# Performance work log

Hardware: AMD Instinct MI355X
Metric: run time of the kernel (lower is better)

Reference implementation:

```python
import jax, jax.numpy as jnp
import numpy as np

NUM_NODES = 100000
NUM_EDGES = 1000000
NUM_REL = 3
NUM_GRAPHS = 512
VOCAB = 10000
EMBED_DIM = 64
HIDDEN_DIM = 64
NUM_CLS = 2


def setup_inputs() -> dict:
    key = jax.random.key(0)
    ks = jax.random.split(key, 10)
    x = jax.random.randint(ks[0], (NUM_NODES,), 0, VOCAB)
    edge_index = jax.random.randint(ks[1], (2, NUM_EDGES), 0, NUM_NODES)
    edge_type = jax.random.randint(ks[2], (NUM_EDGES,), 0, NUM_REL)
    batch = jnp.sort(jax.random.randint(ks[3], (NUM_NODES,), 0, NUM_GRAPHS))
    embed_table = jax.random.normal(ks[4], (VOCAB, EMBED_DIM), dtype=jnp.float32) * 0.02
    embed_table = embed_table.at[0].set(0.0)  # padding_idx=0
    W_rel = jax.random.normal(ks[5], (NUM_REL, EMBED_DIM, HIDDEN_DIM), dtype=jnp.float32) * 0.1
    W_root = jax.random.normal(ks[6], (EMBED_DIM, HIDDEN_DIM), dtype=jnp.float32) * 0.1
    conv_bias = jax.random.normal(ks[7], (HIDDEN_DIM,), dtype=jnp.float32) * 0.01
    lin_W = jax.random.normal(ks[8], (HIDDEN_DIM, NUM_CLS), dtype=jnp.float32) * 0.1
    lin_b = jnp.zeros((NUM_CLS,), dtype=jnp.float32)
    return {"x": x, "edge_index": edge_index, "edge_type": edge_type, "batch": batch,
            "embed_table": embed_table, "W_rel": W_rel, "W_root": W_root,
            "conv_bias": conv_bias, "lin_W": lin_W, "lin_b": lin_b}


def reference(x, edge_index, edge_type, batch, embed_table, W_rel, W_root, conv_bias, lin_W, lin_b):
    # Embedding lookup (padding row already zeroed)
    h = embed_table[x]                                   # [N, D]
    src, dst = edge_index[0], edge_index[1]
    # RGCNConv: root transform + per-relation mean-aggregated neighbor transform
    out = h @ W_root + conv_bias                          # [N, H]
    for r in range(NUM_REL):
        mask = (edge_type == r).astype(h.dtype)           # [E]
        hr = h @ W_rel[r]                                 # [N, H] tiny GEMM
        msg = hr[src] * mask[:, None]                     # [E, H] gather
        agg = jax.ops.segment_sum(msg, dst, num_segments=NUM_NODES)
        cnt = jax.ops.segment_sum(mask, dst, num_segments=NUM_NODES)
        out = out + agg / jnp.maximum(cnt, 1.0)[:, None]
    out = jax.nn.relu(out)
    # global_mean_pool over graph ids
    g_sum = jax.ops.segment_sum(out, batch, num_segments=NUM_GRAPHS)    # [G, H]
    g_cnt = jax.ops.segment_sum(jnp.ones_like(batch, dtype=out.dtype), batch, num_segments=NUM_GRAPHS)
    g_emb = g_sum / jnp.maximum(g_cnt, 1.0)[:, None]
    return g_emb @ lin_W + lin_b                          # [G, num_cls]
```

## Files before the change

### kernel.cpp

```cpp
#include <hip/hip_runtime.h>

#define N_NODES 100000
#define N_EDGES 1000000
#define N_GRAPHS 512
#define VOCAB 10000
#define DIM 64

#define NPB 64
#define NB 1563
#define EPB 4096
#define SB 245
#define BUILD_BLOCKS ((4 * VOCAB) / 16)
#define CAP 1152

typedef unsigned short ushort_t;

static __device__ __forceinline__ ushort_t f2bf(float f) {
    unsigned u = __float_as_uint(f);
    unsigned r = 0x7FFFu + ((u >> 16) & 1u);
    return (ushort_t)((u + r) >> 16);
}
#define BFLO(u) __uint_as_float((u) << 16)
#define BFHI(u) __uint_as_float((u) & 0xFFFF0000u)

__global__ __launch_bounds__(256)
void hist_build(const int* __restrict__ dst, int* __restrict__ bh,
                float* __restrict__ g_sum,
                const float* __restrict__ embed,
                const float* __restrict__ W_rel,
                const float* __restrict__ W_root,
                ushort_t* __restrict__ Tb) {
    if (blockIdx.x < SB) {
        for (int i = blockIdx.x * 256 + threadIdx.x; i < N_GRAPHS * DIM; i += SB * 256)
            g_sum[i] = 0.f;
        __shared__ int h[NB];
        for (int i = threadIdx.x; i < NB; i += 256) h[i] = 0;
        __syncthreads();
        int base = blockIdx.x * EPB;
        int lim  = base + EPB; if (lim > N_EDGES) lim = N_EDGES;
        for (int e = base + threadIdx.x; e < lim; e += 256)
            atomicAdd(&h[dst[e] >> 6], 1);
        __syncthreads();
        for (int i = threadIdx.x; i < NB; i += 256)
            bh[blockIdx.x * NB + i] = h[i];
    } else {
        int tid  = (blockIdx.x - SB) * 256 + threadIdx.x;
        int l    = tid & 63;
        int wave = tid >> 6;
        int sub  = l >> 4;
        int q    = l & 15;
        int row  = wave * 4 + sub;
        int m    = row / VOCAB;
        int v    = row - m * VOCAB;
        const float* W = (m == 0) ? W_root : (W_rel + (size_t)(m - 1) * DIM * DIM);
        float4 e4  = *(const float4*)(embed + (size_t)v * DIM + q * 4);
        float4 acc = {0.f, 0.f, 0.f, 0.f};
#pragma unroll
        for (int kk = 0; kk < 16; ++kk) {
            int srcl = sub * 16 + kk;
            float ex = __shfl(e4.x, srcl, 64);
            float ey = __shfl(e4.y, srcl, 64);
            float ez = __shfl(e4.z, srcl, 64);
            float ew = __shfl(e4.w, srcl, 64);
            const float4 w0 = *(const float4*)(W + (4 * kk + 0) * DIM + q * 4);
            const float4 w1 = *(const float4*)(W + (4 * kk + 1) * DIM + q * 4);
            const float4 w2 = *(const float4*)(W + (4 * kk + 2) * DIM + q * 4);
            const float4 w3 = *(const float4*)(W + (4 * kk + 3) * DIM + q * 4);
            acc.x += ex * w0.x; acc.y += ex * w0.y; acc.z += ex * w0.z; acc.w += ex * w0.w;
            acc.x += ey * w1.x; acc.y += ey * w1.y; acc.z += ey * w1.z; acc.w += ey * w1.w;
            acc.x += ez * w2.x; acc.y += ez * w2.y; acc.z += ez * w2.z; acc.w += ez * w2.w;
            acc.x += ew * w3.x; acc.y += ew * w3.y; acc.z += ew * w3.z; acc.w += ew * w3.w;
        }
        ushort_t* p = Tb + (size_t)row * DIM + q * 4;
        p[0] = f2bf(acc.x); p[1] = f2bf(acc.y);
        p[2] = f2bf(acc.z); p[3] = f2bf(acc.w);
    }
}

__global__ __launch_bounds__(256)
void rowscan(const int* __restrict__ bh, int* __restrict__ loc,
             int* __restrict__ btot) {
    __shared__ int wsum4[4];
    int b = blockIdx.x, t = threadIdx.x;
    int l = t & 63, wv = t >> 6;
    int v = (t < SB) ? bh[t * NB + b] : 0;
    int sc = v;
#pragma unroll
    for (int d = 1; d < 64; d <<= 1) {
        int tt = __shfl_up(sc, d, 64);
        if (l >= d) sc += tt;
    }
    if (l == 63) wsum4[wv] = sc;
    __syncthreads();
    if (t == 0) {
        int a = 0;
#pragma unroll
        for (int k = 0; k < 4; ++k) { int tmp = wsum4[k]; wsum4[k] = a; a += tmp; }
    }
    __syncthreads();
    int excl = sc - v + wsum4[wv];
    if (t < SB) loc[b * SB + t] = excl;
    if (t == 255) btot[b] = excl;
}

__global__ __launch_bounds__(512)
void bucket_scatter(const int* __restrict__ src,
                    const int* __restrict__ dst,
                    const int* __restrict__ etype,
                    const int* __restrict__ x,
                    const int* __restrict__ loc,
                    const int* __restrict__ btot,
                    int* __restrict__ bbase,
                    unsigned* __restrict__ rec) {
    __shared__ int wsum8[8];
    __shared__ int baseh[NB];
    __shared__ int h[NB];
    int t = threadIdx.x;
    int l = t & 63, wv = t >> 6;

    int v0 = (4 * t + 0 < NB) ? btot[4 * t + 0] : 0;
    int v1 = (4 * t + 1 < NB) ? btot[4 * t + 1] : 0;
    int v2 = (4 * t + 2 < NB) ? btot[4 * t + 2] : 0;
    int v3 = (4 * t + 3 < NB) ? btot[4 * t + 3] : 0;
    int lsum = v0 + v1 + v2 + v3;
    int sc = lsum;
#pragma unroll
    for (int d = 1; d < 64; d <<= 1) {
        int tt = __shfl_up(sc, d, 64);
        if (l >= d) sc += tt;
    }
    if (l == 63) wsum8[wv] = sc;
    __syncthreads();
    if (t == 0) {
        int a = 0;
#pragma unroll
        for (int k = 0; k < 8; ++k) { int tmp = wsum8[k]; wsum8[k] = a; a += tmp; }
    }
    __syncthreads();
    int p = sc - lsum + wsum8[wv];
    if (4 * t + 0 < NB) baseh[4 * t + 0] = p; p += v0;
    if (4 * t + 1 < NB) baseh[4 * t + 1] = p; p += v1;
    if (4 * t + 2 < NB) baseh[4 * t + 2] = p; p += v2;
    if (4 * t + 3 < NB) baseh[4 * t + 3] = p;
    __syncthreads();

    if (blockIdx.x == 0) {
        for (int i = t; i < NB; i += 512) bbase[i] = baseh[i];
        if (t == 0) bbase[NB] = N_EDGES;
    }
    for (int i = t; i < NB; i += 512) {
        baseh[i] += loc[i * SB + blockIdx.x];
        h[i] = 0;
    }
    __syncthreads();

    int base = blockIdx.x * EPB;
    int lim  = base + EPB; if (lim > N_EDGES) lim = N_EDGES;
    for (int e = base + t; e < lim; e += 512) {
        int d = dst[e];
        int b = d >> 6;
        int rk = atomicAdd(&h[b], 1);
        unsigned payload = ((unsigned)x[src[e]] << 8)
                         | ((unsigned)(d & 63) << 2)
                         | (unsigned)etype[e];
        rec[baseh[b] + rk] = payload;
    }
}

__global__ __launch_bounds__(256)
void sort_aggregate(const int* __restrict__ x,
                    const int* __restrict__ batch,
                    const int* __restrict__ bbase,
                    const unsigned* __restrict__ rec,
                    const ushort_t* __restrict__ Tb,
                    const float* __restrict__ bias,
                    float* __restrict__ g_sum) {
    __shared__ int cstart[257];
    __shared__ int cur[256];
    __shared__ int wsum4[4];
    __shared__ float inv_sh[256];
    __shared__ unsigned sortedc[CAP];
    __shared__ float rows[NPB * DIM];
    __shared__ float red[256];
    __shared__ int batch_sh[NPB];
    int b = blockIdx.x, t = threadIdx.x;
    int s = bbase[b];
    int e = bbase[b + 1];
    int ne = e - s;
    int nvalid = N_NODES - b * NPB; if (nvalid > NPB) nvalid = NPB;

    cstart[t] = 0;
    if (t < NPB) batch_sh[t] = (t < nvalid) ? batch[b * NPB + t] : -1;
    __syncthreads();
    for (int i = t; i < ne; i += 256)
        atomicAdd(&cstart[rec[s + i] & 0xFFu], 1);
    __syncthreads();
    {
        int l = t & 63, wv = t >> 6;
        int v = cstart[t];
        int sc = v;
#pragma unroll
        for (int d = 1; d < 64; d <<= 1) {
            int tt = __shfl_up(sc, d, 64);
            if (l >= d) sc += tt;
        }
        if (l == 63) wsum4[wv] = sc;
        __syncthreads();
        if (t == 0) {
            int a = 0;
#pragma unroll
            for (int k = 0; k < 4; ++k) { int tmp = wsum4[k]; wsum4[k] = a; a += tmp; }
        }
        __syncthreads();
        int excl = sc - v + wsum4[wv];
        __syncthreads();
        cstart[t] = excl;
        cur[t] = excl;
        if (t == 255) cstart[256] = excl + v;
    }
    __syncthreads();
    inv_sh[t] = 1.f / fmaxf((float)(cstart[t + 1] - cstart[t]), 1.f);
    for (int i = t; i < ne; i += 256) {
        unsigned p = rec[s + i];
        int rk = atomicAdd(&cur[p & 0xFFu], 1);
        sortedc[rk] = p;
    }
    __syncthreads();

    int grp = t >> 3;
    int sl  = t & 7;
    const ushort_t* TbRel = Tb + (size_t)VOCAB * DIM;
#pragma unroll
    for (int nn = 0; nn < 2; ++nn) {
        int n = grp * 2 + nn;
        if (n >= nvalid) continue;
        int node = b * NPB + n;
        int i0 = cstart[n << 2];
        int i1 = cstart[(n + 1) << 2];
        float a0 = 0.f, a1 = 0.f, a2 = 0.f, a3 = 0.f,
              a4 = 0.f, a5 = 0.f, a6 = 0.f, a7 = 0.f;
        int i = i0;
        for (; i + 4 <= i1; i += 4) {
            unsigned c1 = sortedc[i],     c2 = sortedc[i + 1];
            unsigned c3 = sortedc[i + 2], c4 = sortedc[i + 3];
            const uint4 t1 = *(const uint4*)(TbRel +
                ((size_t)(c1 & 3u) * VOCAB + (c1 >> 8)) * DIM + sl * 8);
            const uint4 t2 = *(const uint4*)(TbRel +
                ((size_t)(c2 & 3u) * VOCAB + (c2 >> 8)) * DIM + sl * 8);
            const uint4 t3 = *(const uint4*)(TbRel +
                ((size_t)(c3 & 3u) * VOCAB + (c3 >> 8)) * DIM + sl * 8);
            const uint4 t4 = *(const uint4*)(TbRel +
                ((size_t)(c4 & 3u) * VOCAB + (c4 >> 8)) * DIM + sl * 8);
            float iv1 = inv_sh[c1 & 0xFFu], iv2 = inv_sh[c2 & 0xFFu];
            float iv3 = inv_sh[c3 & 0xFFu], iv4 = inv_sh[c4 & 0xFFu];
            a0 += BFLO(t1.x) * iv1; a1 += BFHI(t1.x) * iv1;
            a2 += BFLO(t1.y) * iv1; a3 += BFHI(t1.y) * iv1;
            a4 += BFLO(t1.z) * iv1; a5 += BFHI(t1.z) * iv1;
            a6 += BFLO(t1.w) * iv1; a7 += BFHI(t1.w) * iv1;
            a0 += BFLO(t2.x) * iv2; a1 += BFHI(t2.x) * iv2;
            a2 += BFLO(t2.y) * iv2; a3 += BFHI(t2.y) * iv2;
            a4 += BFLO(t2.z) * iv2; a5 += BFHI(t2.z) * iv2;
            a6 += BFLO(t2.w) * iv2; a7 += BFHI(t2.w) * iv2;
            a0 += BFLO(t3.x) * iv3; a1 += BFHI(t3.x) * iv3;
            a2 += BFLO(t3.y) * iv3; a3 += BFHI(t3.y) * iv3;
            a4 += BFLO(t3.z) * iv3; a5 += BFHI(t3.z) * iv3;
            a6 += BFLO(t3.w) * iv3; a7 += BFHI(t3.w) * iv3;
            a0 += BFLO(t4.x) * iv4; a1 += BFHI(t4.x) * iv4;
            a2 += BFLO(t4.y) * iv4; a3 += BFHI(t4.y) * iv4;
            a4 += BFLO(t4.z) * iv4; a5 += BFHI(t4.z) * iv4;
            a6 += BFLO(t4.w) * iv4; a7 += BFHI(t4.w) * iv4;
        }
        for (; i < i1; ++i) {
            unsigned c1 = sortedc[i];
            const uint4 t1 = *(const uint4*)(TbRel +
                ((size_t)(c1 & 3u) * VOCAB + (c1 >> 8)) * DIM + sl * 8);
            float iv1 = inv_sh[c1 & 0xFFu];
            a0 += BFLO(t1.x) * iv1; a1 += BFHI(t1.x) * iv1;
            a2 += BFLO(t1.y) * iv1; a3 += BFHI(t1.y) * iv1;
            a4 += BFLO(t1.z) * iv1; a5 += BFHI(t1.z) * iv1;
            a6 += BFLO(t1.w) * iv1; a7 += BFHI(t1.w) * iv1;
        }
        int xv = x[node];
        const uint4 rt = *(const uint4*)(Tb + (size_t)xv * DIM + sl * 8);
        const float4 b0 = *(const float4*)(bias + sl * 8);
        const float4 b1 = *(const float4*)(bias + sl * 8 + 4);
        float* rp = rows + n * DIM + sl * 8;
        rp[0] = fmaxf(BFLO(rt.x) + b0.x + a0, 0.f);
        rp[1] = fmaxf(BFHI(rt.x) + b0.y + a1, 0.f);
        rp[2] = fmaxf(BFLO(rt.y) + b0.z + a2, 0.f);
        rp[3] = fmaxf(BFHI(rt.y) + b0.w + a3, 0.f);
        rp[4] = fmaxf(BFLO(rt.z) + b1.x + a4, 0.f);
        rp[5] = fmaxf(BFHI(rt.z) + b1.y + a5, 0.f);
        rp[6] = fmaxf(BFLO(rt.w) + b1.z + a6, 0.f);
        rp[7] = fmaxf(BFHI(rt.w) + b1.w + a7, 0.f);
    }
    __syncthreads();

    int gmin = batch_sh[0];
    int gmax = batch_sh[nvalid - 1];
    int f  = t & 63;
    int n0 = t >> 6;
    for (int g = gmin; g <= gmax; ++g) {
        float a = 0.f;
        for (int n = n0; n < nvalid; n += 4)
            a += (batch_sh[n] == g) ? rows[n * DIM + f] : 0.f;
        red[t] = a;
        __syncthreads();
        if (t < 64) {
            float tot = red[t] + red[t + 64] + red[t + 128] + red[t + 192];
            if (tot != 0.f) atomicAdd(&g_sum[g * DIM + t], tot);
        }
        __syncthreads();
    }
}

__device__ __forceinline__ int lbound(const int* __restrict__ b, int val) {
    int lo = 0, hi = N_NODES;
    while (lo < hi) {
        int mid = (lo + hi) >> 1;
        if (b[mid] < val) lo = mid + 1; else hi = mid;
    }
    return lo;
}

__global__ __launch_bounds__(64)
void final_linear(const int* __restrict__ batch,
                  const float* __restrict__ g_sum,
                  const float* __restrict__ lin_W,
                  const float* __restrict__ lin_b,
                  float* __restrict__ out) {
    int g = blockIdx.x;
    int l = threadIdx.x;
    int s = lbound(batch, g);
    int e = lbound(batch, g + 1);
    float mean = (e > s) ? g_sum[g * DIM + l] / (float)(e - s) : 0.f;
    float p0 = mean * lin_W[l * 2 + 0];
    float p1 = mean * lin_W[l * 2 + 1];
#pragma unroll
    for (int off2 = 32; off2 > 0; off2 >>= 1) {
        p0 += __shfl_down(p0, off2, 64);
        p1 += __shfl_down(p1, off2, 64);
    }
    if (l == 0) {
        out[g * 2 + 0] = p0 + lin_b[0];
        out[g * 2 + 1] = p1 + lin_b[1];
    }
}

extern "C" void kernel_launch(void* const* d_in, const int* in_sizes, int n_in,
                              void* d_out, int out_size, void* d_ws, size_t ws_size,
                              hipStream_t stream) {
    const int*   x      = (const int*)d_in[0];
    const int*   eidx   = (const int*)d_in[1];
    const int*   etype  = (const int*)d_in[2];
    const int*   batch  = (const int*)d_in[3];
    const float* embed  = (const float*)d_in[4];
    const float* W_rel  = (const float*)d_in[5];
    const float* W_root = (const float*)d_in[6];
    const float* bias   = (const float*)d_in[7];
    const float* lin_W  = (const float*)d_in[8];
    const float* lin_b  = (const float*)d_in[9];
    float* out = (float*)d_out;

    const int* src = eidx;
    const int* dst = eidx + N_EDGES;

    char* ws = (char*)d_ws;
    ushort_t* Tb    = (ushort_t*)(ws);
    unsigned* rec   = (unsigned*)(ws + 5120000);
    int* loc        = (int*)(ws + 9120000);
    int* btot       = (int*)(ws + 10651776);
    int* bbase      = (int*)(ws + 10658048);
    int* bh         = (int*)(ws + 10664320);
    float* g_sum    = (float*)(ws + 12196096);

    hist_build<<<SB + BUILD_BLOCKS, 256, 0, stream>>>(
        dst, bh, g_sum, embed, W_rel, W_root, Tb);

    rowscan<<<NB, 256, 0, stream>>>(bh, loc, btot);

    bucket_scatter<<<SB, 512, 0, stream>>>(src, dst, etype, x, loc, btot, bbase, rec);

    sort_aggregate<<<NB, 256, 0, stream>>>(x, batch, bbase, rec, Tb, bias, g_sum);

    final_linear<<<N_GRAPHS, 64, 0, stream>>>(batch, g_sum, lin_W, lin_b, out);
}
```

Baseline: 84.80 us.

## Precompute edge payloads in histogram pass and widen scatter blocks to 1024

Moves the x[src] gather and payload packing from bucket_scatter into hist_build, where it can overlap with the table-build blocks. The scatter then reads a precomputed payload array and runs with 1024 threads per block instead of 512. The intent is to shorten the serial scatter stage, which has only 245 blocks, by taking the random gather off its critical path. The cost is an extra 4 MB payload write and read through global memory, plus a larger workspace.

```diff
diff --git a/kernel.cpp b/kernel.cpp
--- a/kernel.cpp
+++ b/kernel.cpp
@@ -24,7 +24,12 @@
 #define BFHI(u) __uint_as_float((u) & 0xFFFF0000u)
 
 __global__ __launch_bounds__(256)
-void hist_build(const int* __restrict__ dst, int* __restrict__ bh,
+void hist_build(const int* __restrict__ src,
+                const int* __restrict__ dst,
+                const int* __restrict__ etype,
+                const int* __restrict__ x,
+                int* __restrict__ bh,
+                unsigned* __restrict__ payload,
                 float* __restrict__ g_sum,
                 const float* __restrict__ embed,
                 const float* __restrict__ W_rel,
@@ -38,8 +43,13 @@
         __syncthreads();
         int base = blockIdx.x * EPB;
         int lim  = base + EPB; if (lim > N_EDGES) lim = N_EDGES;
-        for (int e = base + threadIdx.x; e < lim; e += 256)
-            atomicAdd(&h[dst[e] >> 6], 1);
+        for (int e = base + threadIdx.x; e < lim; e += 256) {
+            int d = dst[e];
+            atomicAdd(&h[d >> 6], 1);
+            payload[e] = ((unsigned)x[src[e]] << 8)
+                       | ((unsigned)(d & 63) << 2)
+                       | (unsigned)etype[e];
+        }
         __syncthreads();
         for (int i = threadIdx.x; i < NB; i += 256)
             bh[blockIdx.x * NB + i] = h[i];
@@ -103,52 +113,46 @@
     if (t == 255) btot[b] = excl;
 }
 
-__global__ __launch_bounds__(512)
-void bucket_scatter(const int* __restrict__ src,
-                    const int* __restrict__ dst,
-                    const int* __restrict__ etype,
-                    const int* __restrict__ x,
+__global__ __launch_bounds__(1024)
+void bucket_scatter(const int* __restrict__ dst,
+                    const unsigned* __restrict__ payload,
                     const int* __restrict__ loc,
                     const int* __restrict__ btot,
                     int* __restrict__ bbase,
                     unsigned* __restrict__ rec) {
-    __shared__ int wsum8[8];
+    __shared__ int wsum16[16];
     __shared__ int baseh[NB];
     __shared__ int h[NB];
     int t = threadIdx.x;
     int l = t & 63, wv = t >> 6;
 
-    int v0 = (4 * t + 0 < NB) ? btot[4 * t + 0] : 0;
-    int v1 = (4 * t + 1 < NB) ? btot[4 * t + 1] : 0;
-    int v2 = (4 * t + 2 < NB) ? btot[4 * t + 2] : 0;
-    int v3 = (4 * t + 3 < NB) ? btot[4 * t + 3] : 0;
-    int lsum = v0 + v1 + v2 + v3;
+    int v0 = (2 * t + 0 < NB) ? btot[2 * t + 0] : 0;
+    int v1 = (2 * t + 1 < NB) ? btot[2 * t + 1] : 0;
+    int lsum = v0 + v1;
     int sc = lsum;
 #pragma unroll
     for (int d = 1; d < 64; d <<= 1) {
         int tt = __shfl_up(sc, d, 64);
         if (l >= d) sc += tt;
     }
-    if (l == 63) wsum8[wv] = sc;
+    if (l == 63) wsum16[wv] = sc;
     __syncthreads();
     if (t == 0) {
         int a = 0;
 #pragma unroll
-        for (int k = 0; k < 8; ++k) { int tmp = wsum8[k]; wsum8[k] = a; a += tmp; }
-    }
-    __syncthreads();
-    int p = sc - lsum + wsum8[wv];
-    if (4 * t + 0 < NB) baseh[4 * t + 0] = p; p += v0;
-    if (4 * t + 1 < NB) baseh[4 * t + 1] = p; p += v1;
-    if (4 * t + 2 < NB) baseh[4 * t + 2] = p; p += v2;
-    if (4 * t + 3 < NB) baseh[4 * t + 3] = p;
+        for (int k = 0; k < 16; ++k) { int tmp = wsum16[k]; wsum16[k] = a; a += tmp; }
+    }
+    __syncthreads();
+    int p = sc - lsum + wsum16[wv];
+    if (2 * t + 0 < NB) baseh[2 * t + 0] = p; p += v0;
+    if (2 * t + 1 < NB) baseh[2 * t + 1] = p;
     __syncthreads();
 
     if (blockIdx.x == 0) {
-        for (int i = t; i < NB; i += 512) bbase[i] = baseh[i];
+        for (int i = t; i < NB; i += 1024) bbase[i] = baseh[i];
         if (t == 0) bbase[NB] = N_EDGES;
     }
-    for (int i = t; i < NB; i += 512) {
+    for (int i = t; i < NB; i += 1024) {
         baseh[i] += loc[i * SB + blockIdx.x];
         h[i] = 0;
     }
@@ -156,14 +160,10 @@
 
     int base = blockIdx.x * EPB;
     int lim  = base + EPB; if (lim > N_EDGES) lim = N_EDGES;
-    for (int e = base + t; e < lim; e += 512) {
-        int d = dst[e];
-        int b = d >> 6;
+    for (int e = base + t; e < lim; e += 1024) {
+        int b = dst[e] >> 6;
         int rk = atomicAdd(&h[b], 1);
-        unsigned payload = ((unsigned)x[src[e]] << 8)
-                         | ((unsigned)(d & 63) << 2)
-                         | (unsigned)etype[e];
-        rec[baseh[b] + rk] = payload;
+        rec[baseh[b] + rk] = payload[e];
     }
 }
 
@@ -366,20 +366,21 @@
     const int* dst = eidx + N_EDGES;
 
     char* ws = (char*)d_ws;
-    ushort_t* Tb    = (ushort_t*)(ws);
-    unsigned* rec   = (unsigned*)(ws + 5120000);
-    int* loc        = (int*)(ws + 9120000);
-    int* btot       = (int*)(ws + 10651776);
-    int* bbase      = (int*)(ws + 10658048);
-    int* bh         = (int*)(ws + 10664320);
-    float* g_sum    = (float*)(ws + 12196096);
+    ushort_t* Tb      = (ushort_t*)(ws);
+    unsigned* rec     = (unsigned*)(ws + 5120000);
+    unsigned* payload = (unsigned*)(ws + 9120000);
+    int* loc          = (int*)(ws + 13120000);
+    int* btot         = (int*)(ws + 14651776);
+    int* bbase        = (int*)(ws + 14658048);
+    int* bh           = (int*)(ws + 14664320);
+    float* g_sum      = (float*)(ws + 16196096);
 
     hist_build<<<SB + BUILD_BLOCKS, 256, 0, stream>>>(
-        dst, bh, g_sum, embed, W_rel, W_root, Tb);
+        src, dst, etype, x, bh, payload, g_sum, embed, W_rel, W_root, Tb);
 
     rowscan<<<NB, 256, 0, stream>>>(bh, loc, btot);
 
-    bucket_scatter<<<SB, 512, 0, stream>>>(src, dst, etype, x, loc, btot, bbase, rec);
+    bucket_scatter<<<SB, 1024, 0, stream>>>(dst, payload, loc, btot, bbase, rec);
 
     sort_aggregate<<<NB, 256, 0, stream>>>(x, batch, bbase, rec, Tb, bias, g_sum);
 
```

New measurement: 81.86 us. 1.04x faster.
